# Kernel optimization log

Hardware: AMD Instinct MI355X
Metric: run time of the kernel (lower is better)

The kernel has to match this reference:

```python
import jax, jax.numpy as jnp
import numpy as np

N_HEADS = 16
ROPE_THETA = 10000.0


def _rope_tables(seq_len, head_dim, dtype=jnp.float32):
    half = head_dim // 2
    inv_freq = 1.0 / (ROPE_THETA ** (jnp.arange(0, half, dtype=jnp.float32) / half))
    t = jnp.arange(seq_len, dtype=jnp.float32)
    freqs = jnp.outer(t, inv_freq)  # (S, half)
    return jnp.cos(freqs).astype(dtype), jnp.sin(freqs).astype(dtype)


def _apply_rope(x, cos, sin):
    # x: (B, H, S, hd); cos/sin: (S, hd//2)
    half = x.shape[-1] // 2
    x1, x2 = x[..., :half], x[..., half:]
    c = cos[None, None, :, :]
    s = sin[None, None, :, :]
    return jnp.concatenate([x1 * c - x2 * s, x1 * s + x2 * c], axis=-1)


def setup_inputs() -> dict:
    key = jax.random.key(0)
    k1, k2, k3 = jax.random.split(key, 3)
    B, S, D = 4, 2048, 2048
    hd = D // N_HEADS
    x = jax.random.normal(k1, (B, S, D), dtype=jnp.float32)
    cos, sin = _rope_tables(S, hd)
    w_qkv = jax.random.normal(k2, (D, 3 * D), dtype=jnp.float32) * (D ** -0.5)
    w_out = jax.random.normal(k3, (D, D), dtype=jnp.float32) * (D ** -0.5)
    return {"x": x, "cos": cos, "sin": sin, "w_qkv": w_qkv, "w_out": w_out}


def reference(x, cos, sin, w_qkv, w_out):
    B, S, D = x.shape
    H = N_HEADS
    hd = D // H
    qkv = x @ w_qkv  # (B, S, 3D)
    qkv = qkv.reshape(B, S, 3, H, hd).transpose(2, 0, 3, 1, 4)  # (3, B, H, S, hd)
    q, k, v = qkv[0], qkv[1], qkv[2]
    q = _apply_rope(q, cos, sin)
    k = _apply_rope(k, cos, sin)
    scale = 1.0 / jnp.sqrt(jnp.asarray(hd, dtype=x.dtype))
    scores = jnp.einsum('bhqd,bhkd->bhqk', q, k) * scale  # (B, H, S, S)
    causal = jnp.tril(jnp.ones((S, S), dtype=bool))
    scores = jnp.where(causal[None, None, :, :], scores, jnp.asarray(-1e30, dtype=scores.dtype))
    p = jax.nn.softmax(scores, axis=-1)
    out = jnp.einsum('bhqk,bhkd->bhqd', p, v)  # (B, H, S, hd)
    out = out.transpose(0, 2, 1, 3).reshape(B, S, D)
    return out @ w_out
```

## Files before the change

### kernel.cpp

```cpp
#include <hip/hip_runtime.h>
#include <hip/hip_bf16.h>
#include <stdint.h>

typedef __bf16  bf16x8  __attribute__((ext_vector_type(8)));
typedef float   floatx4 __attribute__((ext_vector_type(4)));

typedef __attribute__((address_space(1))) void gvoid_t;
typedef __attribute__((address_space(3))) void svoid_t;

__device__ __forceinline__ void gld16(ushort* lds, const ushort* g) {
  __builtin_amdgcn_global_load_lds((gvoid_t*)g, (svoid_t*)lds, 16, 0, 0);
}

__device__ __forceinline__ ushort f2bf(float f) {
  union { float f; unsigned u; } v; v.f = f;
  unsigned u = v.u;
  return (ushort)((u + 0x7fffu + ((u >> 16) & 1u)) >> 16);
}
__device__ __forceinline__ float bf2f(ushort h) {
  union { unsigned u; float f; } v; v.u = ((unsigned)h) << 16; return v.f;
}
__device__ __forceinline__ unsigned pk2bf(float a, float b) {
  __hip_bfloat162 h = __float22bfloat162_rn(make_float2(a, b));
  union { __hip_bfloat162 h; unsigned u; } v; v.h = h; return v.u;
}

__global__ __launch_bounds__(256) void cvt_f32_bf16(
    const float* __restrict__ in, ushort* __restrict__ out) {
  int i = blockIdx.x * 256 + threadIdx.x;
  float4 a = ((const float4*)in)[i];
  ushort4 o;
  o.x = f2bf(a.x); o.y = f2bf(a.y); o.z = f2bf(a.z); o.w = f2bf(a.w);
  ((ushort4*)out)[i] = o;
}

__global__ __launch_bounds__(256) void transpose_cvt(
    const float* __restrict__ in, ushort* __restrict__ out, int R, int C) {
  __shared__ ushort tile[64][65];
  const int r0 = blockIdx.y * 64, c0 = blockIdx.x * 64;
  const int t = threadIdx.x;
#pragma unroll
  for (int rep = 0; rep < 16; rep++) {
    int idx = rep * 256 + t;
    int r = idx >> 6, c = idx & 63;
    tile[r][c] = f2bf(in[(size_t)(r0 + r) * C + c0 + c]);
  }
  __syncthreads();
#pragma unroll
  for (int rep = 0; rep < 16; rep++) {
    int idx = rep * 256 + t;
    int r = idx >> 6, c = idx & 63;
    out[(size_t)(c0 + r) * R + r0 + c] = tile[c][r];
  }
}

template <int EPI>
__global__ __launch_bounds__(512, 1) void gemm256(
    const ushort* __restrict__ A, const ushort* __restrict__ Bt,
    float* __restrict__ Cf,
    ushort* __restrict__ C0, ushort* __restrict__ C1, ushort* __restrict__ C2,
    int M, int N, int K) {
  __shared__ __align__(16) ushort As[2][2][256 * 32];
  __shared__ __align__(16) ushort Bs[2][2][256 * 32];
  const int t = threadIdx.x;
  const int lane = t & 63;
  const int w = t >> 6;
  const int l15 = lane & 15;
  const int quad = lane >> 4;
  const int m0 = blockIdx.y * 256;
  const int n0 = blockIdx.x * 256;
  const int wmB = (w >> 2) * 128;
  const int wnB = (w & 3) * 64;

  const int cS = (lane & 3) ^ ((lane >> 3) & 3);
  const size_t aoff = (size_t)(m0 + w * 32 + (lane >> 2)) * K + cS * 8;
  const size_t boff = (size_t)(n0 + w * 32 + (lane >> 2)) * K + cS * 8;

  const ushort* const Ab = &As[0][0][0];
  const ushort* const Bb = &Bs[0][0][0];
  const ushort* aP[4];
  const ushort* bP[4];
#pragma unroll
  for (int m = 0; m < 4; ++m) {
    int r = wmB + m * 16 + l15;
    int c = quad ^ ((r >> 1) & 3);
    aP[m] = Ab + r * 32 + c * 8;
  }
#pragma unroll
  for (int n = 0; n < 4; ++n) {
    int r = wnB + n * 16 + l15;
    int c = quad ^ ((r >> 1) & 3);
    bP[n] = Bb + r * 32 + c * 8;
  }

#define STAGE_A(db, kh, tile)                                                \
  { size_t ko_ = (size_t)(tile) * 64 + (kh) * 32;                            \
    gld16(&As[db][kh][w * 1024],       A + aoff + ko_);                      \
    gld16(&As[db][kh][w * 1024 + 512], A + aoff + 16 * (size_t)K + ko_); }
#define STAGE_B(db, kh, tile)                                                \
  { size_t ko_ = (size_t)(tile) * 64 + (kh) * 32;                            \
    gld16(&Bs[db][kh][w * 1024],       Bt + boff + ko_);                     \
    gld16(&Bs[db][kh][w * 1024 + 512], Bt + boff + 16 * (size_t)K + ko_); }

#define LDA(AF, db, kh, mh)                                                  \
  _Pragma("unroll") for (int m_ = 0; m_ < 4; ++m_)                           \
    AF[m_] = *(const bf16x8*)(aP[m_] +                                       \
                              ((db) * 16384 + (kh) * 8192 + (mh) * 2048));
#define LDB(db, kh)                                                          \
  _Pragma("unroll") for (int n_ = 0; n_ < 4; ++n_)                           \
    bfr[n_] = *(const bf16x8*)(bP[n_] + ((db) * 16384 + (kh) * 8192));

  floatx4 acc[8][4];
  const floatx4 zero = {0.f, 0.f, 0.f, 0.f};
#pragma unroll
  for (int i = 0; i < 8; i++)
#pragma unroll
    for (int j = 0; j < 4; j++) acc[i][j] = zero;

  bf16x8 af0[4], af1[4], bfr[4];

#define PH(db, kh, mh, AFU, AFL, ndb, nkh, nmh, STAGE)                       \
  __builtin_amdgcn_s_barrier();                                              \
  if ((mh) == 0) { LDB(db, kh) }                                             \
  asm volatile("s_waitcnt lgkmcnt(0)" ::: "memory");                         \
  __builtin_amdgcn_sched_barrier(0);                                         \
  __builtin_amdgcn_s_setprio(1);                                             \
  _Pragma("unroll") for (int m_ = 0; m_ < 4; ++m_)                           \
    _Pragma("unroll") for (int n_ = 0; n_ < 4; ++n_)                         \
      acc[(mh) * 4 + m_][n_] = __builtin_amdgcn_mfma_f32_16x16x32_bf16(      \
          AFU[m_], bfr[n_], acc[(mh) * 4 + m_][n_], 0, 0, 0);                \
  __builtin_amdgcn_s_setprio(0);                                             \
  __builtin_amdgcn_sched_barrier(0);                                         \
  LDA(AFL, ndb, nkh, nmh)                                                    \
  STAGE                                                                      \
  asm volatile("s_waitcnt vmcnt(8)" ::: "memory");

  const int NT = K >> 6;
  const int NI = K >> 7;

  STAGE_A(0, 0, 0);
  STAGE_B(0, 0, 0);
  STAGE_A(0, 1, 0);
  STAGE_B(0, 1, 0);
  STAGE_A(1, 0, 1);
  STAGE_B(1, 0, 1);
  asm volatile("s_waitcnt vmcnt(4)" ::: "memory");
  __builtin_amdgcn_s_barrier();
  LDA(af0, 0, 0, 0)

  for (int i = 0; i < NI; ++i) {
    const int t1 = 2 * i + 1;
    int t2 = 2 * i + 2, t3 = 2 * i + 3;
    if (t2 > NT - 1) t2 = NT - 1;
    if (t3 > NT - 1) t3 = NT - 1;
    PH(0, 0, 0, af0, af1, 0, 0, 1, STAGE_A(1, 1, t1))
    PH(0, 0, 1, af1, af0, 0, 1, 0, STAGE_B(1, 1, t1))
    PH(0, 1, 0, af0, af1, 0, 1, 1, STAGE_A(0, 0, t2))
    PH(0, 1, 1, af1, af0, 1, 0, 0, STAGE_B(0, 0, t2))
    PH(1, 0, 0, af0, af1, 1, 0, 1, STAGE_A(0, 1, t2))
    PH(1, 0, 1, af1, af0, 1, 1, 0, STAGE_B(0, 1, t2))
    PH(1, 1, 0, af0, af1, 1, 1, 1, STAGE_A(1, 0, t3))
    PH(1, 1, 1, af1, af0, 0, 0, 0, STAGE_B(1, 0, t3))
  }
  asm volatile("s_waitcnt vmcnt(0)" ::: "memory");

#undef PH
#undef LDA
#undef LDB
#undef STAGE_A
#undef STAGE_B

  if (EPI == 0) {
#pragma unroll
    for (int m = 0; m < 8; ++m)
#pragma unroll
      for (int n = 0; n < 4; ++n)
#pragma unroll
        for (int r = 0; r < 4; ++r) {
          int row = m0 + wmB + m * 16 + quad * 4 + r;
          int col = n0 + wnB + n * 16 + l15;
          Cf[(size_t)row * N + col] = acc[m][n][r];
        }
  } else {
    const int colW = n0 + wnB;
    const int sel = colW >> 11;
    const int h = (colW >> 7) & 15;
    if (sel < 2) {
      ushort* dst = (sel == 0) ? C0 : C1;
#pragma unroll
      for (int m = 0; m < 8; ++m) {
        int rowb = m0 + wmB + m * 16 + quad * 4;
        int b = rowb >> 11, s = rowb & 2047;
#pragma unroll
        for (int n = 0; n < 4; ++n) {
          int d = (colW + n * 16 + l15) & 127;
#pragma unroll
          for (int r = 0; r < 4; ++r)
            dst[((size_t)(b * 16 + h) * 2048 + (s + r)) * 128 + d] =
                f2bf(acc[m][n][r]);
        }
      }
    } else {
#pragma unroll
      for (int m = 0; m < 8; ++m) {
        int rowb = m0 + wmB + m * 16 + quad * 4;
        int b = rowb >> 11, s = rowb & 2047;
#pragma unroll
        for (int n = 0; n < 4; ++n) {
          int d = (colW + n * 16 + l15) & 127;
          ushort4 pk;
          pk.x = f2bf(acc[m][n][0]);
          pk.y = f2bf(acc[m][n][1]);
          pk.z = f2bf(acc[m][n][2]);
          pk.w = f2bf(acc[m][n][3]);
          *(ushort4*)&C2[((size_t)(b * 16 + h) * 128 + d) * 2048 + s] = pk;
        }
      }
    }
  }
}

__global__ __launch_bounds__(256) void rope_kernel(
    ushort* __restrict__ Q, ushort* __restrict__ Kb,
    const float* __restrict__ cosT, const float* __restrict__ sinT) {
  unsigned gid = blockIdx.x * 256u + threadIdx.x;
  int d = gid & 63;
  int s = (gid >> 6) & 2047;
  int bh = (gid >> 17) & 63;
  const bool isK = (gid >> 23) != 0;
  ushort* buf = isK ? Kb : Q;
  const float sc = isK ? 1.0f
                       : 0.08838834764831845f * 1.4426950408889634f;
  size_t base = ((size_t)bh * 2048 + s) * 128;
  float x1 = bf2f(buf[base + d]);
  float x2 = bf2f(buf[base + d + 64]);
  float c = cosT[s * 64 + d];
  float sn = sinT[s * 64 + d];
  buf[base + d] = f2bf((x1 * c - x2 * sn) * sc);
  buf[base + d + 64] = f2bf((x1 * sn + x2 * c) * sc);
}

__global__ __launch_bounds__(512, 4) void attn_kernel(
    const ushort* __restrict__ Q, const ushort* __restrict__ Kb,
    const ushort* __restrict__ VT, ushort* __restrict__ O) {
  __shared__ __align__(16) ushort Ks[2][64 * 128];
  __shared__ __align__(16) ushort Vs[2][128 * 64];
  __shared__ __align__(16) ushort Ps[128 * 64];
  const int t = threadIdx.x, lane = t & 63, w = t >> 6;
  const int l15 = lane & 15, quad = lane >> 4;
  const int bid = blockIdx.x;
  const int tq = 15 - (bid >> 6);
  const int bh = bid & 63;
  const int qrow = tq * 128 + w * 16 + l15;
  const size_t hbase = (size_t)bh * 2048 * 128;
  const float NEGINF = -__builtin_inff();

  const int kr0 = w * 8 + quad, kr1 = w * 8 + 4 + quad;
  const ushort* kS0 = Kb + hbase + (size_t)kr0 * 128 + (l15 ^ (kr0 & 15)) * 8;
  const ushort* kS1 = Kb + hbase + (size_t)kr1 * 128 + (l15 ^ (kr1 & 15)) * 8;
  const int vr0 = w * 16 + (lane >> 3), vr1 = w * 16 + 8 + (lane >> 3);
  const ushort* vS0 = VT + hbase + (size_t)vr0 * 2048 + ((lane & 7) ^ (vr0 & 7)) * 8;
  const ushort* vS1 = VT + hbase + (size_t)vr1 * 2048 + ((lane & 7) ^ (vr1 & 7)) * 8;

  bf16x8 aq[4];
#pragma unroll
  for (int kb = 0; kb < 4; kb++)
    aq[kb] = *(const bf16x8*)&Q[hbase + (size_t)qrow * 128 + kb * 32 + quad * 8];

  float m2 = NEGINF, lsum = 0.f;
  floatx4 oacc[8];
  const floatx4 zero = {0.f, 0.f, 0.f, 0.f};
#pragma unroll
  for (int dj = 0; dj < 8; dj++) oacc[dj] = zero;

  const int ntk = 2 * tq + 2;

#define STAGE(b, tile)                                                \
  { gld16(&Ks[b][(w * 2 + 0) * 512], kS0 + (size_t)(tile) * 8192);    \
    gld16(&Ks[b][(w * 2 + 1) * 512], kS1 + (size_t)(tile) * 8192);    \
    gld16(&Vs[b][(w * 2 + 0) * 512], vS0 + (size_t)(tile) * 64);      \
    gld16(&Vs[b][(w * 2 + 1) * 512], vS1 + (size_t)(tile) * 64); }

  STAGE(0, 0)
  asm volatile("s_waitcnt vmcnt(0)" ::: "memory");
  __builtin_amdgcn_s_barrier();

  int cur = 0;
  for (int tk = 0; tk < ntk; tk++) {
    if (tk + 1 < ntk) STAGE(cur ^ 1, tk + 1)
    const ushort* Kc = &Ks[cur][0];
    const ushort* Vc = &Vs[cur][0];

    floatx4 sacc[4];
#pragma unroll
    for (int j = 0; j < 4; j++) sacc[j] = zero;
#pragma unroll
    for (int kb = 0; kb < 4; kb++) {
#pragma unroll
      for (int j = 0; j < 4; j++) {
        int row = j * 16 + l15;
        int c = (kb * 4 + quad) ^ (row & 15);
        bf16x8 kf = *(const bf16x8*)&Kc[row * 128 + c * 8];
        sacc[j] = __builtin_amdgcn_mfma_f32_16x16x32_bf16(kf, aq[kb], sacc[j],
                                                          0, 0, 0);
      }
    }

    if (tk >= ntk - 2) {
#pragma unroll
      for (int j = 0; j < 4; j++)
#pragma unroll
        for (int r = 0; r < 4; r++) {
          int kcol = tk * 64 + j * 16 + quad * 4 + r;
          if (kcol > qrow) sacc[j][r] = NEGINF;
        }
    }

    float mx = sacc[0][0];
#pragma unroll
    for (int j = 0; j < 4; j++)
#pragma unroll
      for (int r = 0; r < 4; r++) mx = fmaxf(mx, sacc[j][r]);
    mx = fmaxf(mx, __shfl_xor(mx, 16));
    mx = fmaxf(mx, __shfl_xor(mx, 32));
    float mnew = fmaxf(m2, mx);
    float alpha = __builtin_exp2f(m2 - mnew);
    m2 = mnew;
    float rs = 0.f;
#pragma unroll
    for (int j = 0; j < 4; j++)
#pragma unroll
      for (int r = 0; r < 4; r++) {
        float p = __builtin_exp2f(sacc[j][r] - mnew);
        sacc[j][r] = p;
        rs += p;
      }
    rs += __shfl_xor(rs, 16);
    rs += __shfl_xor(rs, 32);
    lsum = lsum * alpha + rs;
    if (__any(alpha < 1.0f)) {
#pragma unroll
      for (int dj = 0; dj < 8; dj++) oacc[dj] *= alpha;
    }

#pragma unroll
    for (int j = 0; j < 4; j++) {
      unsigned lo = pk2bf(sacc[j][0], sacc[j][1]);
      unsigned hi = pk2bf(sacc[j][2], sacc[j][3]);
      int g = j * 2 + (quad >> 1);
      int gp = g ^ (l15 & 7);
      uint2 pv; pv.x = lo; pv.y = hi;
      *(uint2*)&Ps[(w * 16 + l15) * 64 + gp * 8 + (quad & 1) * 4] = pv;
    }

    bf16x8 bp[2];
#pragma unroll
    for (int kk = 0; kk < 2; kk++) {
      int g = kk * 4 + quad;
      int gp = g ^ (l15 & 7);
      bp[kk] = *(const bf16x8*)&Ps[(w * 16 + l15) * 64 + gp * 8];
    }
#pragma unroll
    for (int kk = 0; kk < 2; kk++)
#pragma unroll
      for (int dj = 0; dj < 8; dj++) {
        int rowd = dj * 16 + l15;
        int c = (kk * 4 + quad) ^ (rowd & 7);
        bf16x8 av = *(const bf16x8*)&Vc[rowd * 64 + c * 8];
        oacc[dj] = __builtin_amdgcn_mfma_f32_16x16x32_bf16(av, bp[kk], oacc[dj],
                                                           0, 0, 0);
      }

    asm volatile("s_waitcnt vmcnt(0)" ::: "memory");
    __builtin_amdgcn_s_barrier();
    cur ^= 1;
  }
#undef STAGE

  const int b = bh >> 4, h = bh & 15;
  const float rl = 1.0f / lsum;
  const size_t obase = ((size_t)(b * 2048 + qrow)) * 2048 + h * 128;
#pragma unroll
  for (int dj = 0; dj < 8; dj++) {
    ushort4 pk;
    pk.x = f2bf(oacc[dj][0] * rl);
    pk.y = f2bf(oacc[dj][1] * rl);
    pk.z = f2bf(oacc[dj][2] * rl);
    pk.w = f2bf(oacc[dj][3] * rl);
    *(ushort4*)&O[obase + dj * 16 + quad * 4] = pk;
  }
}

extern "C" void kernel_launch(void* const* d_in, const int* in_sizes, int n_in,
                              void* d_out, int out_size, void* d_ws, size_t ws_size,
                              hipStream_t stream) {
  const float* x    = (const float*)d_in[0];
  const float* cosT = (const float*)d_in[1];
  const float* sinT = (const float*)d_in[2];
  const float* wqkv = (const float*)d_in[3];
  const float* wout = (const float*)d_in[4];
  float* out = (float*)d_out;
  char* ws = (char*)d_ws;

  ushort* xbf   = (ushort*)d_out;
  ushort* wqkvT = (ushort*)(ws);
  ushort* Ob    = (ushort*)(ws);
  ushort* woutT = (ushort*)(ws + 33554432);
  ushort* Qb    = (ushort*)(ws + 41943040);
  ushort* Kbuf  = (ushort*)(ws + 75497472);
  ushort* VTb   = (ushort*)(ws + 109051904);

  cvt_f32_bf16<<<16384, 256, 0, stream>>>(x, xbf);
  transpose_cvt<<<dim3(96, 32), 256, 0, stream>>>(wqkv, wqkvT, 2048, 6144);
  transpose_cvt<<<dim3(32, 32), 256, 0, stream>>>(wout, woutT, 2048, 2048);
  gemm256<1><<<dim3(24, 32), 512, 0, stream>>>(xbf, wqkvT, nullptr,
                                               Qb, Kbuf, VTb, 8192, 6144, 2048);
  rope_kernel<<<65536, 256, 0, stream>>>(Qb, Kbuf, cosT, sinT);
  attn_kernel<<<1024, 512, 0, stream>>>(Qb, Kbuf, VTb, Ob);
  gemm256<0><<<dim3(8, 32), 512, 0, stream>>>(Ob, woutT, out,
                                              nullptr, nullptr, nullptr,
                                              8192, 2048, 2048);
}
```

Baseline: 587.5 us.

## Process two query tiles per attention block with triple-buffered K/V and lazy rescale

```diff
diff --git a/kernel.cpp b/kernel.cpp
--- a/kernel.cpp
+++ b/kernel.cpp
@@ -240,18 +240,19 @@
   buf[base + d + 64] = f2bf((x1 * sn + x2 * c) * sc);
 }
 
-__global__ __launch_bounds__(512, 4) void attn_kernel(
+__global__ __launch_bounds__(512, 1) void attn_kernel(
     const ushort* __restrict__ Q, const ushort* __restrict__ Kb,
     const ushort* __restrict__ VT, ushort* __restrict__ O) {
-  __shared__ __align__(16) ushort Ks[2][64 * 128];
-  __shared__ __align__(16) ushort Vs[2][128 * 64];
-  __shared__ __align__(16) ushort Ps[128 * 64];
+  __shared__ __align__(16) ushort Ks[3][64 * 128];
+  __shared__ __align__(16) ushort Vs[3][128 * 64];
+  __shared__ __align__(16) ushort Ps[2][128 * 64];
   const int t = threadIdx.x, lane = t & 63, w = t >> 6;
   const int l15 = lane & 15, quad = lane >> 4;
   const int bid = blockIdx.x;
-  const int tq = 15 - (bid >> 6);
+  const int tq = 7 - (bid >> 6);
   const int bh = bid & 63;
-  const int qrow = tq * 128 + w * 16 + l15;
+  const int qrowA = tq * 256 + w * 16 + l15;
+  const int qrowB = qrowA + 128;
   const size_t hbase = (size_t)bh * 2048 * 128;
   const float NEGINF = -__builtin_inff();
 
@@ -262,38 +263,43 @@
   const ushort* vS0 = VT + hbase + (size_t)vr0 * 2048 + ((lane & 7) ^ (vr0 & 7)) * 8;
   const ushort* vS1 = VT + hbase + (size_t)vr1 * 2048 + ((lane & 7) ^ (vr1 & 7)) * 8;
 
-  bf16x8 aq[4];
-#pragma unroll
-  for (int kb = 0; kb < 4; kb++)
-    aq[kb] = *(const bf16x8*)&Q[hbase + (size_t)qrow * 128 + kb * 32 + quad * 8];
-
-  float m2 = NEGINF, lsum = 0.f;
-  floatx4 oacc[8];
+  bf16x8 aqa[4], aqb[4];
+#pragma unroll
+  for (int kb = 0; kb < 4; kb++) {
+    aqa[kb] = *(const bf16x8*)&Q[hbase + (size_t)qrowA * 128 + kb * 32 + quad * 8];
+    aqb[kb] = *(const bf16x8*)&Q[hbase + (size_t)qrowB * 128 + kb * 32 + quad * 8];
+  }
+
+  float m2a = NEGINF, lsa = 0.f;
+  float m2b = NEGINF, lsb = 0.f;
+  floatx4 oa[8], ob[8];
   const floatx4 zero = {0.f, 0.f, 0.f, 0.f};
 #pragma unroll
-  for (int dj = 0; dj < 8; dj++) oacc[dj] = zero;
-
-  const int ntk = 2 * tq + 2;
-
-#define STAGE(b, tile)                                                \
-  { gld16(&Ks[b][(w * 2 + 0) * 512], kS0 + (size_t)(tile) * 8192);    \
-    gld16(&Ks[b][(w * 2 + 1) * 512], kS1 + (size_t)(tile) * 8192);    \
-    gld16(&Vs[b][(w * 2 + 0) * 512], vS0 + (size_t)(tile) * 64);      \
-    gld16(&Vs[b][(w * 2 + 1) * 512], vS1 + (size_t)(tile) * 64); }
+  for (int dj = 0; dj < 8; dj++) { oa[dj] = zero; ob[dj] = zero; }
+
+  const int ntk = 4 * tq + 4;
+
+#define STAGE(sl, tile)                                                 \
+  { gld16(&Ks[sl][(w * 2 + 0) * 512], kS0 + (size_t)(tile) * 8192);     \
+    gld16(&Ks[sl][(w * 2 + 1) * 512], kS1 + (size_t)(tile) * 8192);     \
+    gld16(&Vs[sl][(w * 2 + 0) * 512], vS0 + (size_t)(tile) * 64);       \
+    gld16(&Vs[sl][(w * 2 + 1) * 512], vS1 + (size_t)(tile) * 64); }
 
   STAGE(0, 0)
-  asm volatile("s_waitcnt vmcnt(0)" ::: "memory");
+  STAGE(1, 1)
+  asm volatile("s_waitcnt vmcnt(4)" ::: "memory");
   __builtin_amdgcn_s_barrier();
 
-  int cur = 0;
+  int sl = 0, s2 = 2;
   for (int tk = 0; tk < ntk; tk++) {
-    if (tk + 1 < ntk) STAGE(cur ^ 1, tk + 1)
-    const ushort* Kc = &Ks[cur][0];
-    const ushort* Vc = &Vs[cur][0];
-
-    floatx4 sacc[4];
-#pragma unroll
-    for (int j = 0; j < 4; j++) sacc[j] = zero;
+    const bool pf = (tk + 2 < ntk);
+    if (pf) STAGE(s2, tk + 2)
+    const ushort* Kc = &Ks[sl][0];
+    const ushort* Vc = &Vs[sl][0];
+
+    floatx4 sa[4], sb[4];
+#pragma unroll
+    for (int j = 0; j < 4; j++) { sa[j] = zero; sb[j] = zero; }
 #pragma unroll
     for (int kb = 0; kb < 4; kb++) {
 #pragma unroll
@@ -301,64 +307,94 @@
         int row = j * 16 + l15;
         int c = (kb * 4 + quad) ^ (row & 15);
         bf16x8 kf = *(const bf16x8*)&Kc[row * 128 + c * 8];
-        sacc[j] = __builtin_amdgcn_mfma_f32_16x16x32_bf16(kf, aq[kb], sacc[j],
-                                                          0, 0, 0);
-      }
-    }
-
-    if (tk >= ntk - 2) {
+        sa[j] = __builtin_amdgcn_mfma_f32_16x16x32_bf16(kf, aqa[kb], sa[j], 0, 0, 0);
+        sb[j] = __builtin_amdgcn_mfma_f32_16x16x32_bf16(kf, aqb[kb], sb[j], 0, 0, 0);
+      }
+    }
+
+    if (tk >= 4 * tq) {
 #pragma unroll
       for (int j = 0; j < 4; j++)
 #pragma unroll
         for (int r = 0; r < 4; r++) {
           int kcol = tk * 64 + j * 16 + quad * 4 + r;
-          if (kcol > qrow) sacc[j][r] = NEGINF;
-        }
-    }
-
-    float mx = sacc[0][0];
-#pragma unroll
-    for (int j = 0; j < 4; j++)
-#pragma unroll
-      for (int r = 0; r < 4; r++) mx = fmaxf(mx, sacc[j][r]);
-    mx = fmaxf(mx, __shfl_xor(mx, 16));
-    mx = fmaxf(mx, __shfl_xor(mx, 32));
-    float mnew = fmaxf(m2, mx);
-    float alpha = __builtin_exp2f(m2 - mnew);
-    m2 = mnew;
-    float rs = 0.f;
-#pragma unroll
-    for (int j = 0; j < 4; j++)
-#pragma unroll
-      for (int r = 0; r < 4; r++) {
-        float p = __builtin_exp2f(sacc[j][r] - mnew);
-        sacc[j][r] = p;
-        rs += p;
-      }
-    rs += __shfl_xor(rs, 16);
-    rs += __shfl_xor(rs, 32);
-    lsum = lsum * alpha + rs;
-    if (__any(alpha < 1.0f)) {
-#pragma unroll
-      for (int dj = 0; dj < 8; dj++) oacc[dj] *= alpha;
+          if (kcol > qrowA) sa[j][r] = NEGINF;
+        }
+    }
+    if (tk >= 4 * tq + 2) {
+#pragma unroll
+      for (int j = 0; j < 4; j++)
+#pragma unroll
+        for (int r = 0; r < 4; r++) {
+          int kcol = tk * 64 + j * 16 + quad * 4 + r;
+          if (kcol > qrowB) sb[j][r] = NEGINF;
+        }
+    }
+
+    {
+      float mxa = sa[0][0], mxb = sb[0][0];
+#pragma unroll
+      for (int j = 0; j < 4; j++)
+#pragma unroll
+        for (int r = 0; r < 4; r++) {
+          mxa = fmaxf(mxa, sa[j][r]);
+          mxb = fmaxf(mxb, sb[j][r]);
+        }
+      mxa = fmaxf(mxa, __shfl_xor(mxa, 16));
+      mxb = fmaxf(mxb, __shfl_xor(mxb, 16));
+      mxa = fmaxf(mxa, __shfl_xor(mxa, 32));
+      mxb = fmaxf(mxb, __shfl_xor(mxb, 32));
+      if (__any(mxa > m2a + 8.0f)) {
+        float mn = fmaxf(m2a, mxa);
+        float al = __builtin_exp2f(m2a - mn);
+        m2a = mn;
+        lsa *= al;
+#pragma unroll
+        for (int dj = 0; dj < 8; dj++) oa[dj] *= al;
+      }
+      if (__any(mxb > m2b + 8.0f)) {
+        float mn = fmaxf(m2b, mxb);
+        float al = __builtin_exp2f(m2b - mn);
+        m2b = mn;
+        lsb *= al;
+#pragma unroll
+        for (int dj = 0; dj < 8; dj++) ob[dj] *= al;
+      }
+      float rsa = 0.f, rsb = 0.f;
+#pragma unroll
+      for (int j = 0; j < 4; j++)
+#pragma unroll
+        for (int r = 0; r < 4; r++) {
+          float pa = __builtin_exp2f(sa[j][r] - m2a);
+          float pb = __builtin_exp2f(sb[j][r] - m2b);
+          sa[j][r] = pa; sb[j][r] = pb;
+          rsa += pa; rsb += pb;
+        }
+      lsa += rsa;
+      lsb += rsb;
     }
 
 #pragma unroll
     for (int j = 0; j < 4; j++) {
-      unsigned lo = pk2bf(sacc[j][0], sacc[j][1]);
-      unsigned hi = pk2bf(sacc[j][2], sacc[j][3]);
       int g = j * 2 + (quad >> 1);
       int gp = g ^ (l15 & 7);
-      uint2 pv; pv.x = lo; pv.y = hi;
-      *(uint2*)&Ps[(w * 16 + l15) * 64 + gp * 8 + (quad & 1) * 4] = pv;
-    }
-
-    bf16x8 bp[2];
+      int off = (w * 16 + l15) * 64 + gp * 8 + (quad & 1) * 4;
+      uint2 pva, pvb;
+      pva.x = pk2bf(sa[j][0], sa[j][1]);
+      pva.y = pk2bf(sa[j][2], sa[j][3]);
+      pvb.x = pk2bf(sb[j][0], sb[j][1]);
+      pvb.y = pk2bf(sb[j][2], sb[j][3]);
+      *(uint2*)&Ps[0][off] = pva;
+      *(uint2*)&Ps[1][off] = pvb;
+    }
+
+    bf16x8 bpa[2], bpb[2];
 #pragma unroll
     for (int kk = 0; kk < 2; kk++) {
       int g = kk * 4 + quad;
       int gp = g ^ (l15 & 7);
-      bp[kk] = *(const bf16x8*)&Ps[(w * 16 + l15) * 64 + gp * 8];
+      bpa[kk] = *(const bf16x8*)&Ps[0][(w * 16 + l15) * 64 + gp * 8];
+      bpb[kk] = *(const bf16x8*)&Ps[1][(w * 16 + l15) * 64 + gp * 8];
     }
 #pragma unroll
     for (int kk = 0; kk < 2; kk++)
@@ -367,27 +403,43 @@
         int rowd = dj * 16 + l15;
         int c = (kk * 4 + quad) ^ (rowd & 7);
         bf16x8 av = *(const bf16x8*)&Vc[rowd * 64 + c * 8];
-        oacc[dj] = __builtin_amdgcn_mfma_f32_16x16x32_bf16(av, bp[kk], oacc[dj],
-                                                           0, 0, 0);
-      }
-
-    asm volatile("s_waitcnt vmcnt(0)" ::: "memory");
+        oa[dj] = __builtin_amdgcn_mfma_f32_16x16x32_bf16(av, bpa[kk], oa[dj], 0, 0, 0);
+        ob[dj] = __builtin_amdgcn_mfma_f32_16x16x32_bf16(av, bpb[kk], ob[dj], 0, 0, 0);
+      }
+
+    if (pf) {
+      asm volatile("s_waitcnt vmcnt(4)" ::: "memory");
+    } else {
+      asm volatile("s_waitcnt vmcnt(0)" ::: "memory");
+    }
     __builtin_amdgcn_s_barrier();
-    cur ^= 1;
+    sl = (sl == 2) ? 0 : sl + 1;
+    s2 = (s2 == 2) ? 0 : s2 + 1;
   }
 #undef STAGE
 
   const int b = bh >> 4, h = bh & 15;
-  const float rl = 1.0f / lsum;
-  const size_t obase = ((size_t)(b * 2048 + qrow)) * 2048 + h * 128;
+  lsa += __shfl_xor(lsa, 16);
+  lsb += __shfl_xor(lsb, 16);
+  lsa += __shfl_xor(lsa, 32);
+  lsb += __shfl_xor(lsb, 32);
+  const float rla = 1.0f / lsa;
+  const float rlb = 1.0f / lsb;
+  const size_t obaseA = ((size_t)(b * 2048 + qrowA)) * 2048 + h * 128;
+  const size_t obaseB = ((size_t)(b * 2048 + qrowB)) * 2048 + h * 128;
 #pragma unroll
   for (int dj = 0; dj < 8; dj++) {
-    ushort4 pk;
-    pk.x = f2bf(oacc[dj][0] * rl);
-    pk.y = f2bf(oacc[dj][1] * rl);
-    pk.z = f2bf(oacc[dj][2] * rl);
-    pk.w = f2bf(oacc[dj][3] * rl);
-    *(ushort4*)&O[obase + dj * 16 + quad * 4] = pk;
+    ushort4 pka, pkb;
+    pka.x = f2bf(oa[dj][0] * rla);
+    pka.y = f2bf(oa[dj][1] * rla);
+    pka.z = f2bf(oa[dj][2] * rla);
+    pka.w = f2bf(oa[dj][3] * rla);
+    pkb.x = f2bf(ob[dj][0] * rlb);
+    pkb.y = f2bf(ob[dj][1] * rlb);
+    pkb.z = f2bf(ob[dj][2] * rlb);
+    pkb.w = f2bf(ob[dj][3] * rlb);
+    *(ushort4*)&O[obaseA + dj * 16 + quad * 4] = pka;
+    *(ushort4*)&O[obaseB + dj * 16 + quad * 4] = pkb;
   }
 }
 
@@ -416,7 +468,7 @@
   gemm256<1><<<dim3(24, 32), 512, 0, stream>>>(xbf, wqkvT, nullptr,
                                                Qb, Kbuf, VTb, 8192, 6144, 2048);
   rope_kernel<<<65536, 256, 0, stream>>>(Qb, Kbuf, cosT, sinT);
-  attn_kernel<<<1024, 512, 0, stream>>>(Qb, Kbuf, VTb, Ob);
+  attn_kernel<<<512, 512, 0, stream>>>(Qb, Kbuf, VTb, Ob);
   gemm256<0><<<dim3(8, 32), 512, 0, stream>>>(Ob, woutT, out,
                                               nullptr, nullptr, nullptr,
                                               8192, 2048, 2048);
```

After: 586.6 us. No clear change (-0.1%).
